# Optimization experiments

Measured on AMD Instinct MI355X. Metric: run time of the kernel, lower is better.

## Reference

```python
import jax, jax.numpy as jnp
import numpy as np

FEAT = 128
SCALE = FEAT ** -0.5

def _linear(x, W, b):
    # torch nn.Linear: y = x @ W.T + b, W: [out, in]
    return jnp.einsum('bnd,od->bno', x, W) + b

def setup_inputs() -> dict:
    key = jax.random.key(0)
    ks = jax.random.split(key, 12)
    B, N1, N2 = 2, 4096, 32768
    inp = {
        'sparse_xyz':  jax.random.normal(ks[0], (B, N1, 3),    dtype=jnp.float32),
        'sparse_feat': jax.random.normal(ks[1], (B, N1, FEAT), dtype=jnp.float32),
        'dense_xyz':   jax.random.normal(ks[2], (B, N2, 3),    dtype=jnp.float32),
        'dense_feat':  jax.random.normal(ks[3], (B, N2, FEAT), dtype=jnp.float32),
    }
    s_in = (FEAT + 3) ** -0.5  # torch Linear default init bound ~ 1/sqrt(in)
    s_f = FEAT ** -0.5
    inp['Wq'] = jax.random.uniform(ks[4], (FEAT, FEAT + 3), jnp.float32, -s_in, s_in)
    inp['bq'] = jax.random.uniform(ks[5], (FEAT,), jnp.float32, -s_in, s_in)
    inp['Wk'] = jax.random.uniform(ks[6], (FEAT, FEAT + 3), jnp.float32, -s_in, s_in)
    inp['bk'] = jax.random.uniform(ks[7], (FEAT,), jnp.float32, -s_in, s_in)
    inp['Wv'] = jax.random.uniform(ks[8], (FEAT, FEAT), jnp.float32, -s_f, s_f)
    inp['bv'] = jax.random.uniform(ks[9], (FEAT,), jnp.float32, -s_f, s_f)
    inp['Wo'] = jax.random.uniform(ks[10], (FEAT, FEAT), jnp.float32, -s_f, s_f)
    inp['bo'] = jax.random.uniform(ks[11], (FEAT,), jnp.float32, -s_f, s_f)
    return inp

def reference(sparse_xyz, sparse_feat, dense_xyz, dense_feat,
              Wq, bq, Wk, bk, Wv, bv, Wo, bo):
    # Projections
    Q = _linear(jnp.concatenate([dense_xyz, dense_feat], axis=-1), Wq, bq)   # [B,N2,F]
    K = _linear(jnp.concatenate([sparse_xyz, sparse_feat], axis=-1), Wk, bk) # [B,N1,F]
    V = _linear(sparse_feat, Wv, bv)                                          # [B,N1,F]
    # Attention scores with euclidean distance penalty (torch.cdist, p=2)
    scores = jnp.einsum('bqf,bkf->bqk', Q, K) * SCALE                         # [B,N2,N1]
    sq = (jnp.sum(dense_xyz**2, -1)[:, :, None]
          + jnp.sum(sparse_xyz**2, -1)[:, None, :]
          - 2.0 * jnp.einsum('bqd,bkd->bqk', dense_xyz, sparse_xyz))
    dist = jnp.sqrt(jnp.maximum(sq, 1e-12))
    attn = jax.nn.softmax(scores - 0.5 * dist, axis=-1)                       # [B,N2,N1]
    propagated = jnp.einsum('bqk,bkf->bqf', attn, V)                          # [B,N2,F]
    return _linear(propagated + dense_feat, Wo, bo)
```

## Files before the change

### kernel.cpp

```cpp
#include <hip/hip_runtime.h>
#include <stdint.h>

#define NB 2
#define N1 4096
#define N2 32768
#define DD 128
#define KT 32
#define NTILES (N1 / KT)
static constexpr float SCLE = 0.1275174306f;
static constexpr float CNEG = -0.7213475204444817f;
static constexpr float THR  = 11.5415603f;

typedef float f32x16 __attribute__((ext_vector_type(16)));
typedef __bf16 bf16x8v __attribute__((ext_vector_type(8)));
typedef __bf16 bf16x2v __attribute__((ext_vector_type(2)));
typedef unsigned int u32;
typedef unsigned short u16;

union FragU { uint4 u; bf16x8v b; };

__device__ __forceinline__ u16 f2bf(float f) {
  __bf16 h = (__bf16)f;
  return __builtin_bit_cast(u16, h);
}
__device__ __forceinline__ u32 pk2(float lo, float hi) {
  bf16x2v v; v[0] = (__bf16)lo; v[1] = (__bf16)hi;
  return __builtin_bit_cast(u32, v);
}
__device__ __forceinline__ float bfhi(float f) {
  return (float)(__bf16)f;
}
__device__ __forceinline__ f32x16 MFMA(uint4 a, uint4 b, const f32x16& c) {
  FragU A, B; A.u = a; B.u = b;
  return __builtin_amdgcn_mfma_f32_32x32x16_bf16(A.b, B.b, c, 0, 0, 0);
}
__device__ __forceinline__ uint4 packhi8(float4 a, float4 b) {
  return make_uint4(pk2(a.x, a.y), pk2(a.z, a.w), pk2(b.x, b.y), pk2(b.z, b.w));
}
__device__ __forceinline__ uint4 packlo8(float4 a, float4 b) {
  return make_uint4(pk2(a.x - bfhi(a.x), a.y - bfhi(a.y)),
                    pk2(a.z - bfhi(a.z), a.w - bfhi(a.w)),
                    pk2(b.x - bfhi(b.x), b.y - bfhi(b.y)),
                    pk2(b.z - bfhi(b.z), b.w - bfhi(b.w)));
}
__device__ __forceinline__ uint4 conv8(float a0, float a1, float a2, float a3,
                                       float a4, float a5, float a6, float a7, int h) {
  u32 A0 = pk2(a0, a1), A1 = pk2(a2, a3);
  u32 B0 = pk2(a4, a5), B1 = pk2(a6, a7);
  u32 A0s = (u32)__shfl_xor((int)A0, 32);
  u32 A1s = (u32)__shfl_xor((int)A1, 32);
  u32 B0s = (u32)__shfl_xor((int)B0, 32);
  u32 B1s = (u32)__shfl_xor((int)B1, 32);
  return h ? make_uint4(B0s, B1s, B0, B1) : make_uint4(A0, A1, A0s, A1s);
}

__global__ __launch_bounds__(256) void prep_kv(
    const float* __restrict__ sxyz, const float* __restrict__ sfeat,
    const float* __restrict__ Wk, const float* __restrict__ bk,
    const float* __restrict__ Wv, const float* __restrict__ bv,
    u16* __restrict__ Kws, u16* __restrict__ VTws, u16* __restrict__ EKws) {
  const int tid = threadIdx.x;
  const int l = tid & 63, w = tid >> 6, h = l >> 5, ln = l & 31;
  const int b = blockIdx.x >> 5;
  const int kb = (blockIdx.x & 31) * 128;
  const int key = kb + w * 32 + ln;
  const size_t frow = (size_t)(b * N1 + key) * DD;

  uint4 xf[8];
#pragma unroll
  for (int s = 0; s < 8; ++s) {
    const float4* fp = (const float4*)(sfeat + frow + s * 16 + h * 8);
    xf[s] = packhi8(fp[0], fp[1]);
  }
  const float* xp = sxyz + (size_t)(b * N1 + key) * 3;
  float sx = xp[0], sy = xp[1], sz = xp[2];
  uint4 x8 = h ? make_uint4(0, 0, 0, 0)
               : make_uint4(pk2(sx, sy), pk2(sz, 0.f), 0u, 0u);

  f32x16 kacc[4], vacc[4];
#pragma unroll
  for (int ot = 0; ot < 4; ++ot)
#pragma unroll
    for (int r = 0; r < 16; ++r) {
      int o = (r & 3) + 8 * (r >> 2) + 4 * h + 32 * ot;
      kacc[ot][r] = bk[o];
      vacc[ot][r] = bv[o];
    }

#pragma unroll
  for (int ot = 0; ot < 4; ++ot) {
    const int out = ln + 32 * ot;
    const float* wkr = Wk + (size_t)out * 131;
    const float* wvr = Wv + (size_t)out * DD;
#pragma unroll
    for (int s = 0; s < 8; ++s) {
      const float* p = wkr + 3 + s * 16 + h * 8;
      uint4 wa = make_uint4(pk2(p[0], p[1]), pk2(p[2], p[3]),
                            pk2(p[4], p[5]), pk2(p[6], p[7]));
      kacc[ot] = MFMA(wa, xf[s], kacc[ot]);
      const float4* q = (const float4*)(wvr + s * 16 + h * 8);
      vacc[ot] = MFMA(packhi8(q[0], q[1]), xf[s], vacc[ot]);
    }
    uint4 w8 = h ? make_uint4(0, 0, 0, 0)
                 : make_uint4(pk2(wkr[0], wkr[1]), pk2(wkr[2], 0.f), 0u, 0u);
    kacc[ot] = MFMA(w8, x8, kacc[ot]);
  }

#pragma unroll
  for (int ot = 0; ot < 4; ++ot) {
#pragma unroll
    for (int rq = 0; rq < 4; ++rq) {
      uint2 kv;
      kv.x = pk2(kacc[ot][rq * 4 + 0], kacc[ot][rq * 4 + 1]);
      kv.y = pk2(kacc[ot][rq * 4 + 2], kacc[ot][rq * 4 + 3]);
      *(uint2*)&Kws[(size_t)(b * N1 + key) * DD + ot * 32 + rq * 8 + h * 4] = kv;
    }
#pragma unroll
    for (int r = 0; r < 16; ++r) {
      int o = (r & 3) + 8 * (r >> 2) + 4 * h + 32 * ot;
      VTws[(size_t)(b * DD + o) * N1 + key] = f2bf(vacc[ot][r]);
    }
  }

  if (tid < 128) {
    int k2i = kb + tid;
    const float* xq = sxyz + (size_t)(b * N1 + k2i) * 3;
    float x = xq[0], y = xq[1], z = xq[2];
    float k2 = x * x + y * y + z * z;
    float xh = bfhi(x), xl = x - xh;
    float yh = bfhi(y), yl = y - yh;
    float zh = bfhi(z), zl = z - zh;
    float k2h = bfhi(k2), k2l = k2 - k2h;
    uint4 e0 = make_uint4(pk2(xh, xl), pk2(xh, yh), pk2(yl, yh), pk2(zh, zl));
    uint4 e1 = make_uint4(pk2(zh, k2h), pk2(k2l, 0.f), 0u, 0u);
    uint4* dst = (uint4*)&EKws[(size_t)(b * N1 + k2i) * 16];
    dst[0] = e0;
    dst[1] = e1;
  }
}

__global__ __launch_bounds__(256, 2) void attn_fwd(
    const float* __restrict__ dxyz, const float* __restrict__ dfeat,
    const float* __restrict__ Wq, const float* __restrict__ bq,
    const float* __restrict__ Wo, const float* __restrict__ bo,
    const u16* __restrict__ Kws, const u16* __restrict__ VTws,
    const u16* __restrict__ EKws, float* __restrict__ out) {
  __shared__ __align__(16) u16 sm[8192];

  const int tid = threadIdx.x;
  const int l = tid & 63, w = tid >> 6, h = l >> 5, ln = l & 31;
  const int b = blockIdx.x >> 8;
  const int qb = (blockIdx.x & 255) * 128;
  const int qi = qb + w * 32 + ln;
  const int bN1 = b * N1;
  const size_t qrow = (size_t)(b * N2 + qi);

  const float* xp = dxyz + qrow * 3;
  const float qx = xp[0], qy = xp[1], qz = xp[2];
  const float q2 = qx * qx + qy * qy + qz * qz;
  float xh = bfhi(qx), xl = qx - xh, yh = bfhi(qy), yl = qy - yh, zh = bfhi(qz), zl = qz - zh;
  const uint4 eq = h ? make_uint4(pk2(-2.f * zl, 1.f), pk2(1.f, 0.f), 0u, 0u)
                     : make_uint4(pk2(-2.f * xh, -2.f * xh), pk2(-2.f * xl, -2.f * yh),
                                  pk2(-2.f * yh, -2.f * yl), pk2(-2.f * zh, -2.f * zh));

  uint4 qf[8];
  {
    uint4 xf[8];
#pragma unroll
    for (int s = 0; s < 8; ++s) {
      const float4* fp = (const float4*)(dfeat + qrow * DD + s * 16 + h * 8);
      xf[s] = packhi8(fp[0], fp[1]);
    }
    uint4 x8 = h ? make_uint4(0, 0, 0, 0)
                 : make_uint4(pk2(qx, qy), pk2(qz, 0.f), 0u, 0u);
    f32x16 qt[4];
#pragma unroll
    for (int ot = 0; ot < 4; ++ot) {
#pragma unroll
      for (int r = 0; r < 16; ++r)
        qt[ot][r] = SCLE * bq[(r & 3) + 8 * (r >> 2) + 4 * h + 32 * ot];
      const float* wqr = Wq + (size_t)(ln + 32 * ot) * 131;
#pragma unroll
      for (int s = 0; s < 8; ++s) {
        const float* p = wqr + 3 + s * 16 + h * 8;
        uint4 wa = make_uint4(pk2(SCLE * p[0], SCLE * p[1]), pk2(SCLE * p[2], SCLE * p[3]),
                              pk2(SCLE * p[4], SCLE * p[5]), pk2(SCLE * p[6], SCLE * p[7]));
        qt[ot] = MFMA(wa, xf[s], qt[ot]);
      }
      uint4 w8 = h ? make_uint4(0, 0, 0, 0)
                   : make_uint4(pk2(SCLE * wqr[0], SCLE * wqr[1]), pk2(SCLE * wqr[2], 0.f), 0u, 0u);
      qt[ot] = MFMA(w8, x8, qt[ot]);
    }
#pragma unroll
    for (int s = 0; s < 8; ++s) {
      const f32x16& c = qt[s >> 1];
      const int br = (s & 1) * 8;
      qf[s] = conv8(c[br + 0], c[br + 1], c[br + 2], c[br + 3],
                    c[br + 4], c[br + 5], c[br + 6], c[br + 7], h);
    }
  }

  f32x16 oacc[4];
#pragma unroll
  for (int ft = 0; ft < 4; ++ft)
#pragma unroll
    for (int r = 0; r < 16; ++r) oacc[ft][r] = 0.f;
  float m = -1e30f, lsum = 0.f;

  const int kr = tid >> 4, kd = tid & 15;
  const int vr = tid >> 2, vd = tid & 3;
  const int kswz = (kd ^ (kr & 7)) * 8;
  const int vswz = (vd ^ ((vr >> 1) & 3)) * 8;
  const int vx = (ln >> 1) & 3;
  const u16* Kb = Kws + (size_t)bN1 * DD;
  const u16* Vb = VTws + (size_t)b * DD * N1;
  uint4 k0g, k1g, v0g, v1g;

#define LOADT(kt)                                                            \
  do {                                                                       \
    k0g = *(const uint4*)&Kb[(size_t)((kt) + kr) * DD + kd * 8];             \
    k1g = *(const uint4*)&Kb[(size_t)((kt) + kr + 16) * DD + kd * 8];        \
    v0g = *(const uint4*)&Vb[(size_t)vr * N1 + (kt) + vd * 8];               \
    v1g = *(const uint4*)&Vb[(size_t)(vr + 64) * N1 + (kt) + vd * 8];        \
  } while (0)
#define WRITET()                                                             \
  do {                                                                       \
    *(uint4*)&sm[kr * 128 + kswz] = k0g;                                     \
    *(uint4*)&sm[(kr + 16) * 128 + kswz] = k1g;                              \
    *(uint4*)&sm[4096 + vr * 32 + vswz] = v0g;                               \
    *(uint4*)&sm[4096 + (vr + 64) * 32 + vswz] = v1g;                        \
  } while (0)

  LOADT(0);
  WRITET();
  uint4 ek = *(const uint4*)&EKws[(size_t)(bN1 + ln) * 16 + h * 8];

  for (int t = 0; t < NTILES; ++t) {
    __syncthreads();
    const bool more = (t + 1 < NTILES);
    if (more) LOADT((t + 1) * KT);

    f32x16 sacc;
#pragma unroll
    for (int r = 0; r < 16; ++r) sacc[r] = q2;
    sacc = MFMA(ek, eq, sacc);
#pragma unroll
    for (int r = 0; r < 16; ++r)
      sacc[r] = CNEG * __builtin_amdgcn_sqrtf(fmaxf(sacc[r], 0.f));

    {
      const int ktn = more ? (t + 1) * KT : 0;
      ek = *(const uint4*)&EKws[(size_t)(bN1 + ktn + ln) * 16 + h * 8];
    }

    __builtin_amdgcn_s_setprio(1);
#pragma unroll
    for (int kk = 0; kk < 8; ++kk) {
      const uint4 ka = *(const uint4*)&sm[ln * 128 + (((2 * kk + h) ^ (ln & 7)) * 8)];
      sacc = MFMA(ka, qf[kk], sacc);
    }
    __builtin_amdgcn_s_setprio(0);

    float t0 = fmaxf(sacc[0], sacc[1]),   t1 = fmaxf(sacc[2], sacc[3]);
    float t2 = fmaxf(sacc[4], sacc[5]),   t3 = fmaxf(sacc[6], sacc[7]);
    float t4 = fmaxf(sacc[8], sacc[9]),   t5 = fmaxf(sacc[10], sacc[11]);
    float t6 = fmaxf(sacc[12], sacc[13]), t7 = fmaxf(sacc[14], sacc[15]);
    float tmax = fmaxf(fmaxf(fmaxf(t0, t1), fmaxf(t2, t3)),
                       fmaxf(fmaxf(t4, t5), fmaxf(t6, t7)));
    tmax = fmaxf(tmax, __shfl_xor(tmax, 32));
    if (!__all(tmax <= m + THR)) {
      float nm = fmaxf(m, tmax);
      float f = __builtin_amdgcn_exp2f(m - nm);
      lsum *= f;
#pragma unroll
      for (int ft = 0; ft < 4; ++ft)
#pragma unroll
        for (int r = 0; r < 16; ++r) oacc[ft][r] *= f;
      m = nm;
    }
#pragma unroll
    for (int r = 0; r < 16; ++r) sacc[r] = __builtin_amdgcn_exp2f(sacc[r] - m);
    {
      float s0 = sacc[0] + sacc[1],   s1 = sacc[2] + sacc[3];
      float s2 = sacc[4] + sacc[5],   s3 = sacc[6] + sacc[7];
      float s4 = sacc[8] + sacc[9],   s5 = sacc[10] + sacc[11];
      float s6 = sacc[12] + sacc[13], s7 = sacc[14] + sacc[15];
      lsum += (s0 + s1) + (s2 + s3) + ((s4 + s5) + (s6 + s7));
    }

    const uint4 pf0 = conv8(sacc[0], sacc[1], sacc[2], sacc[3],
                            sacc[4], sacc[5], sacc[6], sacc[7], h);
    const uint4 pf1 = conv8(sacc[8], sacc[9], sacc[10], sacc[11],
                            sacc[12], sacc[13], sacc[14], sacc[15], h);
    __builtin_amdgcn_s_setprio(1);
#pragma unroll
    for (int ft = 0; ft < 4; ++ft) {
      const int rr = 32 * ft + ln;
      const uint4 va0 = *(const uint4*)&sm[4096 + rr * 32 + ((h ^ vx) * 8)];
      oacc[ft] = MFMA(va0, pf0, oacc[ft]);
      const uint4 va1 = *(const uint4*)&sm[4096 + rr * 32 + (((2 + h) ^ vx) * 8)];
      oacc[ft] = MFMA(va1, pf1, oacc[ft]);
    }
    __builtin_amdgcn_s_setprio(0);

    __syncthreads();
    if (more) WRITET();
  }
#undef LOADT
#undef WRITET

  lsum += __shfl_xor(lsum, 32);
  const float inv = 1.f / lsum;
#pragma unroll
  for (int ft = 0; ft < 4; ++ft)
#pragma unroll
    for (int r = 0; r < 16; ++r) oacc[ft][r] *= inv;

  f32x16 oc[4];
#pragma unroll
  for (int ot = 0; ot < 4; ++ot)
#pragma unroll
    for (int r = 0; r < 16; ++r)
      oc[ot][r] = bo[(r & 3) + 8 * (r >> 2) + 4 * h + 32 * ot];

#pragma unroll
  for (int s = 0; s < 8; ++s) {
    const f32x16& c = oacc[s >> 1];
    const int br = (s & 1) * 8;
    const uint4 pb = conv8(c[br + 0], c[br + 1], c[br + 2], c[br + 3],
                           c[br + 4], c[br + 5], c[br + 6], c[br + 7], h);
    const float4* fp = (const float4*)(dfeat + qrow * DD + s * 16 + h * 8);
    const float4 fa = fp[0], fb = fp[1];
    const uint4 fh = packhi8(fa, fb);
    const uint4 fl = packlo8(fa, fb);
#pragma unroll
    for (int ot = 0; ot < 4; ++ot) {
      const float4* wp = (const float4*)(Wo + (size_t)(ln + 32 * ot) * DD + s * 16 + h * 8);
      const float4 wa = wp[0], wb = wp[1];
      const uint4 wh = packhi8(wa, wb);
      const uint4 wl = packlo8(wa, wb);
      oc[ot] = MFMA(wh, pb, oc[ot]);
      oc[ot] = MFMA(wh, fh, oc[ot]);
      oc[ot] = MFMA(wh, fl, oc[ot]);
      oc[ot] = MFMA(wl, fh, oc[ot]);
    }
  }

  float* orow = out + qrow * DD;
#pragma unroll
  for (int ot = 0; ot < 4; ++ot)
#pragma unroll
    for (int rq = 0; rq < 4; ++rq)
      *(float4*)&orow[ot * 32 + rq * 8 + h * 4] =
          make_float4(oc[ot][rq * 4 + 0], oc[ot][rq * 4 + 1],
                      oc[ot][rq * 4 + 2], oc[ot][rq * 4 + 3]);
}

extern "C" void kernel_launch(void* const* d_in, const int* in_sizes, int n_in,
                              void* d_out, int out_size, void* d_ws, size_t ws_size,
                              hipStream_t stream) {
  const float* sxyz = (const float*)d_in[0];
  const float* sfeat = (const float*)d_in[1];
  const float* dxyz = (const float*)d_in[2];
  const float* dfeat = (const float*)d_in[3];
  const float* Wq = (const float*)d_in[4];
  const float* bq = (const float*)d_in[5];
  const float* Wk = (const float*)d_in[6];
  const float* bk = (const float*)d_in[7];
  const float* Wv = (const float*)d_in[8];
  const float* bv = (const float*)d_in[9];
  const float* Wo = (const float*)d_in[10];
  const float* bo = (const float*)d_in[11];

  u16* Kws = (u16*)d_ws;
  u16* VTws = Kws + (size_t)NB * N1 * DD;
  u16* EKws = VTws + (size_t)NB * DD * N1;

  prep_kv<<<dim3(64), dim3(256), 0, stream>>>(sxyz, sfeat, Wk, bk, Wv, bv, Kws, VTws, EKws);
  attn_fwd<<<dim3(512), dim3(256), 0, stream>>>(dxyz, dfeat, Wq, bq, Wo, bo,
                                                Kws, VTws, EKws, (float*)d_out);
}
```

Before: 330.6 us.

## Process two query groups per wave to reuse K/V LDS tiles

```diff
diff --git a/kernel.cpp b/kernel.cpp
--- a/kernel.cpp
+++ b/kernel.cpp
@@ -27,8 +27,9 @@
   bf16x2v v; v[0] = (__bf16)lo; v[1] = (__bf16)hi;
   return __builtin_bit_cast(u32, v);
 }
-__device__ __forceinline__ float bfhi(float f) {
-  return (float)(__bf16)f;
+__device__ __forceinline__ float bfhi(float f) { return (float)(__bf16)f; }
+__device__ __forceinline__ float m3(float a, float b, float c) {
+  return fmaxf(fmaxf(a, b), c);
 }
 __device__ __forceinline__ f32x16 MFMA(uint4 a, uint4 b, const f32x16& c) {
   FragU A, B; A.u = a; B.u = b;
@@ -61,9 +62,9 @@
     u16* __restrict__ Kws, u16* __restrict__ VTws, u16* __restrict__ EKws) {
   const int tid = threadIdx.x;
   const int l = tid & 63, w = tid >> 6, h = l >> 5, ln = l & 31;
-  const int b = blockIdx.x >> 5;
-  const int kb = (blockIdx.x & 31) * 128;
-  const int key = kb + w * 32 + ln;
+  const int b = blockIdx.x >> 7;
+  const int kb = (blockIdx.x & 127) * 32;
+  const int key = kb + ln;
   const size_t frow = (size_t)(b * N1 + key) * DD;
 
   uint4 xf[8];
@@ -77,52 +78,46 @@
   uint4 x8 = h ? make_uint4(0, 0, 0, 0)
                : make_uint4(pk2(sx, sy), pk2(sz, 0.f), 0u, 0u);
 
-  f32x16 kacc[4], vacc[4];
-#pragma unroll
-  for (int ot = 0; ot < 4; ++ot)
-#pragma unroll
-    for (int r = 0; r < 16; ++r) {
-      int o = (r & 3) + 8 * (r >> 2) + 4 * h + 32 * ot;
-      kacc[ot][r] = bk[o];
-      vacc[ot][r] = bv[o];
-    }
-
-#pragma unroll
-  for (int ot = 0; ot < 4; ++ot) {
-    const int out = ln + 32 * ot;
-    const float* wkr = Wk + (size_t)out * 131;
-    const float* wvr = Wv + (size_t)out * DD;
-#pragma unroll
-    for (int s = 0; s < 8; ++s) {
-      const float* p = wkr + 3 + s * 16 + h * 8;
-      uint4 wa = make_uint4(pk2(p[0], p[1]), pk2(p[2], p[3]),
-                            pk2(p[4], p[5]), pk2(p[6], p[7]));
-      kacc[ot] = MFMA(wa, xf[s], kacc[ot]);
-      const float4* q = (const float4*)(wvr + s * 16 + h * 8);
-      vacc[ot] = MFMA(packhi8(q[0], q[1]), xf[s], vacc[ot]);
-    }
+  f32x16 kacc, vacc;
+#pragma unroll
+  for (int r = 0; r < 16; ++r) {
+    int o = (r & 3) + 8 * (r >> 2) + 4 * h + 32 * w;
+    kacc[r] = bk[o];
+    vacc[r] = bv[o];
+  }
+
+  const int outd = ln + 32 * w;
+  const float* wkr = Wk + (size_t)outd * 131;
+  const float* wvr = Wv + (size_t)outd * DD;
+#pragma unroll
+  for (int s = 0; s < 8; ++s) {
+    const float* p = wkr + 3 + s * 16 + h * 8;
+    uint4 wa = make_uint4(pk2(p[0], p[1]), pk2(p[2], p[3]),
+                          pk2(p[4], p[5]), pk2(p[6], p[7]));
+    kacc = MFMA(wa, xf[s], kacc);
+    const float4* q = (const float4*)(wvr + s * 16 + h * 8);
+    vacc = MFMA(packhi8(q[0], q[1]), xf[s], vacc);
+  }
+  {
     uint4 w8 = h ? make_uint4(0, 0, 0, 0)
                  : make_uint4(pk2(wkr[0], wkr[1]), pk2(wkr[2], 0.f), 0u, 0u);
-    kacc[ot] = MFMA(w8, x8, kacc[ot]);
-  }
-
-#pragma unroll
-  for (int ot = 0; ot < 4; ++ot) {
-#pragma unroll
-    for (int rq = 0; rq < 4; ++rq) {
-      uint2 kv;
-      kv.x = pk2(kacc[ot][rq * 4 + 0], kacc[ot][rq * 4 + 1]);
-      kv.y = pk2(kacc[ot][rq * 4 + 2], kacc[ot][rq * 4 + 3]);
-      *(uint2*)&Kws[(size_t)(b * N1 + key) * DD + ot * 32 + rq * 8 + h * 4] = kv;
-    }
-#pragma unroll
-    for (int r = 0; r < 16; ++r) {
-      int o = (r & 3) + 8 * (r >> 2) + 4 * h + 32 * ot;
-      VTws[(size_t)(b * DD + o) * N1 + key] = f2bf(vacc[ot][r]);
-    }
-  }
-
-  if (tid < 128) {
+    kacc = MFMA(w8, x8, kacc);
+  }
+
+#pragma unroll
+  for (int rq = 0; rq < 4; ++rq) {
+    uint2 kv;
+    kv.x = pk2(kacc[rq * 4 + 0], kacc[rq * 4 + 1]);
+    kv.y = pk2(kacc[rq * 4 + 2], kacc[rq * 4 + 3]);
+    *(uint2*)&Kws[(size_t)(b * N1 + key) * DD + w * 32 + rq * 8 + h * 4] = kv;
+  }
+#pragma unroll
+  for (int r = 0; r < 16; ++r) {
+    int o = (r & 3) + 8 * (r >> 2) + 4 * h + 32 * w;
+    VTws[(size_t)(b * DD + o) * N1 + key] = f2bf(vacc[r]);
+  }
+
+  if (tid < 32) {
     int k2i = kb + tid;
     const float* xq = sxyz + (size_t)(b * N1 + k2i) * 3;
     float x = xq[0], y = xq[1], z = xq[2];
@@ -132,14 +127,14 @@
     float zh = bfhi(z), zl = z - zh;
     float k2h = bfhi(k2), k2l = k2 - k2h;
     uint4 e0 = make_uint4(pk2(xh, xl), pk2(xh, yh), pk2(yl, yh), pk2(zh, zl));
-    uint4 e1 = make_uint4(pk2(zh, k2h), pk2(k2l, 0.f), 0u, 0u);
+    uint4 e1 = make_uint4(pk2(zh, k2h), pk2(k2l, 1.f), pk2(1.f, 0.f), 0u);
     uint4* dst = (uint4*)&EKws[(size_t)(b * N1 + k2i) * 16];
     dst[0] = e0;
     dst[1] = e1;
   }
 }
 
-__global__ __launch_bounds__(256, 2) void attn_fwd(
+__global__ __launch_bounds__(256, 1) void attn_fwd(
     const float* __restrict__ dxyz, const float* __restrict__ dfeat,
     const float* __restrict__ Wq, const float* __restrict__ bq,
     const float* __restrict__ Wo, const float* __restrict__ bo,
@@ -149,63 +144,84 @@
 
   const int tid = threadIdx.x;
   const int l = tid & 63, w = tid >> 6, h = l >> 5, ln = l & 31;
-  const int b = blockIdx.x >> 8;
-  const int qb = (blockIdx.x & 255) * 128;
-  const int qi = qb + w * 32 + ln;
+  const int b = blockIdx.x >> 7;
+  const int qb = (blockIdx.x & 127) * 256;
   const int bN1 = b * N1;
-  const size_t qrow = (size_t)(b * N2 + qi);
-
-  const float* xp = dxyz + qrow * 3;
-  const float qx = xp[0], qy = xp[1], qz = xp[2];
-  const float q2 = qx * qx + qy * qy + qz * qz;
-  float xh = bfhi(qx), xl = qx - xh, yh = bfhi(qy), yl = qy - yh, zh = bfhi(qz), zl = qz - zh;
-  const uint4 eq = h ? make_uint4(pk2(-2.f * zl, 1.f), pk2(1.f, 0.f), 0u, 0u)
-                     : make_uint4(pk2(-2.f * xh, -2.f * xh), pk2(-2.f * xl, -2.f * yh),
-                                  pk2(-2.f * yh, -2.f * yl), pk2(-2.f * zh, -2.f * zh));
-
-  uint4 qf[8];
+  size_t qrow[2];
+  qrow[0] = (size_t)(b * N2 + qb + w * 64 + ln);
+  qrow[1] = qrow[0] + 32;
+
+  f32x16 zf;
+#pragma unroll
+  for (int r = 0; r < 16; ++r) zf[r] = 0.f;
+
+  uint4 eq[2];
+  float qx[2], qy[2], qz[2];
+#pragma unroll
+  for (int g = 0; g < 2; ++g) {
+    const float* xp = dxyz + qrow[g] * 3;
+    float x = xp[0], y = xp[1], z = xp[2];
+    float q2 = x * x + y * y + z * z;
+    float xh = bfhi(x), xl = x - xh, yh = bfhi(y), yl = y - yh, zh = bfhi(z), zl = z - zh;
+    float q2h = bfhi(q2), q2l = q2 - q2h;
+    eq[g] = h ? make_uint4(pk2(-2.f * zl, 1.f), pk2(1.f, q2h), pk2(q2l, 0.f), 0u)
+              : make_uint4(pk2(-2.f * xh, -2.f * xh), pk2(-2.f * xl, -2.f * yh),
+                           pk2(-2.f * yh, -2.f * yl), pk2(-2.f * zh, -2.f * zh));
+    qx[g] = x; qy[g] = y; qz[g] = z;
+  }
+
+  uint4 qf[2][8];
   {
-    uint4 xf[8];
-#pragma unroll
-    for (int s = 0; s < 8; ++s) {
-      const float4* fp = (const float4*)(dfeat + qrow * DD + s * 16 + h * 8);
-      xf[s] = packhi8(fp[0], fp[1]);
-    }
-    uint4 x8 = h ? make_uint4(0, 0, 0, 0)
-                 : make_uint4(pk2(qx, qy), pk2(qz, 0.f), 0u, 0u);
-    f32x16 qt[4];
+    uint4 xf[2][8], x8[2];
+#pragma unroll
+    for (int g = 0; g < 2; ++g) {
+#pragma unroll
+      for (int s = 0; s < 8; ++s) {
+        const float4* fp = (const float4*)(dfeat + qrow[g] * DD + s * 16 + h * 8);
+        xf[g][s] = packhi8(fp[0], fp[1]);
+      }
+      x8[g] = h ? make_uint4(0, 0, 0, 0)
+                : make_uint4(pk2(qx[g], qy[g]), pk2(qz[g], 0.f), 0u, 0u);
+    }
 #pragma unroll
     for (int ot = 0; ot < 4; ++ot) {
-#pragma unroll
-      for (int r = 0; r < 16; ++r)
-        qt[ot][r] = SCLE * bq[(r & 3) + 8 * (r >> 2) + 4 * h + 32 * ot];
+      f32x16 qt[2];
+#pragma unroll
+      for (int r = 0; r < 16; ++r) {
+        float bqv = SCLE * bq[(r & 3) + 8 * (r >> 2) + 4 * h + 32 * ot];
+        qt[0][r] = bqv; qt[1][r] = bqv;
+      }
       const float* wqr = Wq + (size_t)(ln + 32 * ot) * 131;
 #pragma unroll
       for (int s = 0; s < 8; ++s) {
         const float* p = wqr + 3 + s * 16 + h * 8;
         uint4 wa = make_uint4(pk2(SCLE * p[0], SCLE * p[1]), pk2(SCLE * p[2], SCLE * p[3]),
                               pk2(SCLE * p[4], SCLE * p[5]), pk2(SCLE * p[6], SCLE * p[7]));
-        qt[ot] = MFMA(wa, xf[s], qt[ot]);
+        qt[0] = MFMA(wa, xf[0][s], qt[0]);
+        qt[1] = MFMA(wa, xf[1][s], qt[1]);
       }
       uint4 w8 = h ? make_uint4(0, 0, 0, 0)
                    : make_uint4(pk2(SCLE * wqr[0], SCLE * wqr[1]), pk2(SCLE * wqr[2], 0.f), 0u, 0u);
-      qt[ot] = MFMA(w8, x8, qt[ot]);
-    }
-#pragma unroll
-    for (int s = 0; s < 8; ++s) {
-      const f32x16& c = qt[s >> 1];
-      const int br = (s & 1) * 8;
-      qf[s] = conv8(c[br + 0], c[br + 1], c[br + 2], c[br + 3],
-                    c[br + 4], c[br + 5], c[br + 6], c[br + 7], h);
-    }
-  }
-
-  f32x16 oacc[4];
-#pragma unroll
-  for (int ft = 0; ft < 4; ++ft)
-#pragma unroll
-    for (int r = 0; r < 16; ++r) oacc[ft][r] = 0.f;
-  float m = -1e30f, lsum = 0.f;
+      qt[0] = MFMA(w8, x8[0], qt[0]);
+      qt[1] = MFMA(w8, x8[1], qt[1]);
+#pragma unroll
+      for (int g = 0; g < 2; ++g) {
+        qf[g][2 * ot] = conv8(qt[g][0], qt[g][1], qt[g][2], qt[g][3],
+                              qt[g][4], qt[g][5], qt[g][6], qt[g][7], h);
+        qf[g][2 * ot + 1] = conv8(qt[g][8], qt[g][9], qt[g][10], qt[g][11],
+                                  qt[g][12], qt[g][13], qt[g][14], qt[g][15], h);
+      }
+    }
+  }
+
+  f32x16 oacc[2][4];
+#pragma unroll
+  for (int g = 0; g < 2; ++g)
+#pragma unroll
+    for (int ft = 0; ft < 4; ++ft)
+#pragma unroll
+      for (int r = 0; r < 16; ++r) oacc[g][ft][r] = 0.f;
+  float m[2] = {-1e30f, -1e30f}, lsum[2] = {0.f, 0.f};
 
   const int kr = tid >> 4, kd = tid & 15;
   const int vr = tid >> 2, vd = tid & 3;
@@ -240,13 +256,14 @@
     const bool more = (t + 1 < NTILES);
     if (more) LOADT((t + 1) * KT);
 
-    f32x16 sacc;
-#pragma unroll
-    for (int r = 0; r < 16; ++r) sacc[r] = q2;
-    sacc = MFMA(ek, eq, sacc);
-#pragma unroll
-    for (int r = 0; r < 16; ++r)
-      sacc[r] = CNEG * __builtin_amdgcn_sqrtf(fmaxf(sacc[r], 0.f));
+    f32x16 sacc[2];
+    sacc[0] = MFMA(ek, eq[0], zf);
+    sacc[1] = MFMA(ek, eq[1], zf);
+#pragma unroll
+    for (int g = 0; g < 2; ++g)
+#pragma unroll
+      for (int r = 0; r < 16; ++r)
+        sacc[g][r] = CNEG * __builtin_amdgcn_sqrtf(fmaxf(sacc[g][r], 0.f));
 
     {
       const int ktn = more ? (t + 1) * KT : 0;
@@ -257,49 +274,57 @@
 #pragma unroll
     for (int kk = 0; kk < 8; ++kk) {
       const uint4 ka = *(const uint4*)&sm[ln * 128 + (((2 * kk + h) ^ (ln & 7)) * 8)];
-      sacc = MFMA(ka, qf[kk], sacc);
+      sacc[0] = MFMA(ka, qf[0][kk], sacc[0]);
+      sacc[1] = MFMA(ka, qf[1][kk], sacc[1]);
     }
     __builtin_amdgcn_s_setprio(0);
 
-    float t0 = fmaxf(sacc[0], sacc[1]),   t1 = fmaxf(sacc[2], sacc[3]);
-    float t2 = fmaxf(sacc[4], sacc[5]),   t3 = fmaxf(sacc[6], sacc[7]);
-    float t4 = fmaxf(sacc[8], sacc[9]),   t5 = fmaxf(sacc[10], sacc[11]);
-    float t6 = fmaxf(sacc[12], sacc[13]), t7 = fmaxf(sacc[14], sacc[15]);
-    float tmax = fmaxf(fmaxf(fmaxf(t0, t1), fmaxf(t2, t3)),
-                       fmaxf(fmaxf(t4, t5), fmaxf(t6, t7)));
-    tmax = fmaxf(tmax, __shfl_xor(tmax, 32));
-    if (!__all(tmax <= m + THR)) {
-      float nm = fmaxf(m, tmax);
-      float f = __builtin_amdgcn_exp2f(m - nm);
-      lsum *= f;
-#pragma unroll
-      for (int ft = 0; ft < 4; ++ft)
-#pragma unroll
-        for (int r = 0; r < 16; ++r) oacc[ft][r] *= f;
-      m = nm;
-    }
-#pragma unroll
-    for (int r = 0; r < 16; ++r) sacc[r] = __builtin_amdgcn_exp2f(sacc[r] - m);
-    {
-      float s0 = sacc[0] + sacc[1],   s1 = sacc[2] + sacc[3];
-      float s2 = sacc[4] + sacc[5],   s3 = sacc[6] + sacc[7];
-      float s4 = sacc[8] + sacc[9],   s5 = sacc[10] + sacc[11];
-      float s6 = sacc[12] + sacc[13], s7 = sacc[14] + sacc[15];
-      lsum += (s0 + s1) + (s2 + s3) + ((s4 + s5) + (s6 + s7));
-    }
-
-    const uint4 pf0 = conv8(sacc[0], sacc[1], sacc[2], sacc[3],
-                            sacc[4], sacc[5], sacc[6], sacc[7], h);
-    const uint4 pf1 = conv8(sacc[8], sacc[9], sacc[10], sacc[11],
-                            sacc[12], sacc[13], sacc[14], sacc[15], h);
+    uint4 pf[2][2];
+#pragma unroll
+    for (int g = 0; g < 2; ++g) {
+      float a0 = m3(sacc[g][0], sacc[g][1], sacc[g][2]);
+      float a1 = m3(sacc[g][3], sacc[g][4], sacc[g][5]);
+      float a2 = m3(sacc[g][6], sacc[g][7], sacc[g][8]);
+      float a3 = m3(sacc[g][9], sacc[g][10], sacc[g][11]);
+      float a4 = m3(sacc[g][12], sacc[g][13], sacc[g][14]);
+      float tmax = fmaxf(m3(m3(a0, a1, a2), a3, a4), sacc[g][15]);
+      tmax = fmaxf(tmax, __shfl_xor(tmax, 32));
+      if (!__all(tmax <= m[g] + THR)) {
+        float nm = fmaxf(m[g], tmax);
+        float f = __builtin_amdgcn_exp2f(m[g] - nm);
+        lsum[g] *= f;
+#pragma unroll
+        for (int ft = 0; ft < 4; ++ft)
+#pragma unroll
+          for (int r = 0; r < 16; ++r) oacc[g][ft][r] *= f;
+        m[g] = nm;
+      }
+#pragma unroll
+      for (int r = 0; r < 16; ++r)
+        sacc[g][r] = __builtin_amdgcn_exp2f(sacc[g][r] - m[g]);
+      {
+        float s0 = sacc[g][0] + sacc[g][1],   s1 = sacc[g][2] + sacc[g][3];
+        float s2 = sacc[g][4] + sacc[g][5],   s3 = sacc[g][6] + sacc[g][7];
+        float s4 = sacc[g][8] + sacc[g][9],   s5 = sacc[g][10] + sacc[g][11];
+        float s6 = sacc[g][12] + sacc[g][13], s7 = sacc[g][14] + sacc[g][15];
+        lsum[g] += (s0 + s1) + (s2 + s3) + ((s4 + s5) + (s6 + s7));
+      }
+      pf[g][0] = conv8(sacc[g][0], sacc[g][1], sacc[g][2], sacc[g][3],
+                       sacc[g][4], sacc[g][5], sacc[g][6], sacc[g][7], h);
+      pf[g][1] = conv8(sacc[g][8], sacc[g][9], sacc[g][10], sacc[g][11],
+                       sacc[g][12], sacc[g][13], sacc[g][14], sacc[g][15], h);
+    }
+
     __builtin_amdgcn_s_setprio(1);
 #pragma unroll
     for (int ft = 0; ft < 4; ++ft) {
       const int rr = 32 * ft + ln;
       const uint4 va0 = *(const uint4*)&sm[4096 + rr * 32 + ((h ^ vx) * 8)];
-      oacc[ft] = MFMA(va0, pf0, oacc[ft]);
+      oacc[0][ft] = MFMA(va0, pf[0][0], oacc[0][ft]);
+      oacc[1][ft] = MFMA(va0, pf[1][0], oacc[1][ft]);
       const uint4 va1 = *(const uint4*)&sm[4096 + rr * 32 + (((2 + h) ^ vx) * 8)];
-      oacc[ft] = MFMA(va1, pf1, oacc[ft]);
+      oacc[0][ft] = MFMA(va1, pf[0][1], oacc[0][ft]);
+      oacc[1][ft] = MFMA(va1, pf[1][1], oacc[1][ft]);
     }
     __builtin_amdgcn_s_setprio(0);
 
@@ -309,51 +334,66 @@
 #undef LOADT
 #undef WRITET
 
-  lsum += __shfl_xor(lsum, 32);
-  const float inv = 1.f / lsum;
-#pragma unroll
-  for (int ft = 0; ft < 4; ++ft)
-#pragma unroll
-    for (int r = 0; r < 16; ++r) oacc[ft][r] *= inv;
-
-  f32x16 oc[4];
-#pragma unroll
-  for (int ot = 0; ot < 4; ++ot)
-#pragma unroll
-    for (int r = 0; r < 16; ++r)
-      oc[ot][r] = bo[(r & 3) + 8 * (r >> 2) + 4 * h + 32 * ot];
+#pragma unroll
+  for (int g = 0; g < 2; ++g) {
+    lsum[g] += __shfl_xor(lsum[g], 32);
+    const float inv = 1.f / lsum[g];
+#pragma unroll
+    for (int ft = 0; ft < 4; ++ft)
+#pragma unroll
+      for (int r = 0; r < 16; ++r) oacc[g][ft][r] *= inv;
+  }
+
+  f32x16 oc[2][4];
+#pragma unroll
+  for (int g = 0; g < 2; ++g)
+#pragma unroll
+    for (int ot = 0; ot < 4; ++ot)
+#pragma unroll
+      for (int r = 0; r < 16; ++r)
+        oc[g][ot][r] = bo[(r & 3) + 8 * (r >> 2) + 4 * h + 32 * ot];
 
 #pragma unroll
   for (int s = 0; s < 8; ++s) {
-    const f32x16& c = oacc[s >> 1];
-    const int br = (s & 1) * 8;
-    const uint4 pb = conv8(c[br + 0], c[br + 1], c[br + 2], c[br + 3],
-                           c[br + 4], c[br + 5], c[br + 6], c[br + 7], h);
-    const float4* fp = (const float4*)(dfeat + qrow * DD + s * 16 + h * 8);
-    const float4 fa = fp[0], fb = fp[1];
-    const uint4 fh = packhi8(fa, fb);
-    const uint4 fl = packlo8(fa, fb);
+    uint4 pb[2], fh[2], fl[2];
+#pragma unroll
+    for (int g = 0; g < 2; ++g) {
+      const f32x16& c = oacc[g][s >> 1];
+      const int br = (s & 1) * 8;
+      pb[g] = conv8(c[br + 0], c[br + 1], c[br + 2], c[br + 3],
+                    c[br + 4], c[br + 5], c[br + 6], c[br + 7], h);
+      const float4* fp = (const float4*)(dfeat + qrow[g] * DD + s * 16 + h * 8);
+      const float4 fa = fp[0], fb = fp[1];
+      fh[g] = packhi8(fa, fb);
+      fl[g] = packlo8(fa, fb);
+    }
 #pragma unroll
     for (int ot = 0; ot < 4; ++ot) {
       const float4* wp = (const float4*)(Wo + (size_t)(ln + 32 * ot) * DD + s * 16 + h * 8);
       const float4 wa = wp[0], wb = wp[1];
       const uint4 wh = packhi8(wa, wb);
       const uint4 wl = packlo8(wa, wb);
-      oc[ot] = MFMA(wh, pb, oc[ot]);
-      oc[ot] = MFMA(wh, fh, oc[ot]);
-      oc[ot] = MFMA(wh, fl, oc[ot]);
-      oc[ot] = MFMA(wl, fh, oc[ot]);
-    }
-  }
-
-  float* orow = out + qrow * DD;
-#pragma unroll
-  for (int ot = 0; ot < 4; ++ot)
-#pragma unroll
-    for (int rq = 0; rq < 4; ++rq)
-      *(float4*)&orow[ot * 32 + rq * 8 + h * 4] =
-          make_float4(oc[ot][rq * 4 + 0], oc[ot][rq * 4 + 1],
-                      oc[ot][rq * 4 + 2], oc[ot][rq * 4 + 3]);
+#pragma unroll
+      for (int g = 0; g < 2; ++g) {
+        oc[g][ot] = MFMA(wh, pb[g], oc[g][ot]);
+        oc[g][ot] = MFMA(wh, fh[g], oc[g][ot]);
+        oc[g][ot] = MFMA(wh, fl[g], oc[g][ot]);
+        oc[g][ot] = MFMA(wl, fh[g], oc[g][ot]);
+      }
+    }
+  }
+
+#pragma unroll
+  for (int g = 0; g < 2; ++g) {
+    float* orow = out + qrow[g] * DD;
+#pragma unroll
+    for (int ot = 0; ot < 4; ++ot)
+#pragma unroll
+      for (int rq = 0; rq < 4; ++rq)
+        *(float4*)&orow[ot * 32 + rq * 8 + h * 4] =
+            make_float4(oc[g][ot][rq * 4 + 0], oc[g][ot][rq * 4 + 1],
+                        oc[g][ot][rq * 4 + 2], oc[g][ot][rq * 4 + 3]);
+  }
 }
 
 extern "C" void kernel_launch(void* const* d_in, const int* in_sizes, int n_in,
@@ -376,7 +416,8 @@
   u16* VTws = Kws + (size_t)NB * N1 * DD;
   u16* EKws = VTws + (size_t)NB * DD * N1;
 
-  prep_kv<<<dim3(64), dim3(256), 0, stream>>>(sxyz, sfeat, Wk, bk, Wv, bv, Kws, VTws, EKws);
-  attn_fwd<<<dim3(512), dim3(256), 0, stream>>>(dxyz, dfeat, Wq, bq, Wo, bo,
-                                                Kws, VTws, EKws, (float*)d_out);
-}
+  prep_kv<<<dim3(NB * 128), dim3(256), 0, stream>>>(sxyz, sfeat, Wk, bk, Wv, bv,
+                                                    Kws, VTws, EKws);
+  attn_fwd<<<dim3(NB * 128), dim3(256), 0, stream>>>(dxyz, dfeat, Wq, bq, Wo, bo,
+                                                     Kws, VTws, EKws, (float*)d_out);
+}
```

Result: slower. 383.1 us (+15.9%).
